# Kernel optimization log

Measured on AMD Instinct MI355X. Metric: run time of the kernel, lower is better.

## Reference

```python
import jax, jax.numpy as jnp
from jax import lax
import numpy as np
jax.config.update("jax_enable_x64", True)

NUM_CLASSES = 4
RADIUS = 3
POOL = 2
HALF_D = RADIUS ** 3  # 27
_CLIP_MIN = 1e-06
_POS_ALPHA = 0.0005


def setup_inputs() -> dict:
    key = jax.random.key(0)
    k1, k2 = jax.random.split(key)
    logits = jax.random.normal(k1, (2, NUM_CLASSES, 96, 96, 96), dtype=jnp.float32)
    labels = jax.random.randint(k2, (2, 96, 96, 96), 0, NUM_CLASSES).astype(jnp.int64)
    return {"logits": logits, "labels": labels}


def _max_pool3d(x):
    # kernel=stride=POOL over the last three dims of [N,C,H,W,Z]
    return lax.reduce_window(x, -jnp.inf, lax.max,
                             (1, 1, POOL, POOL, POOL), (1, 1, POOL, POOL, POOL), 'VALID')


def _get_pair_vectors(x):
    # x: [N,C,H,W,Z] -> [N,C,HALF_D, (H-R+1)*(W-R+1)*(Z-R+1)] of shifted overlapping copies
    n, c, h, w, z = x.shape
    nh, nw, nz = h - (RADIUS - 1), w - (RADIUS - 1), z - (RADIUS - 1)
    shifts = [x[:, :, i:i + nh, j:j + nw, k:k + nz]
              for i in range(RADIUS) for j in range(RADIUS) for k in range(RADIUS)]
    return jnp.stack(shifts, axis=2).reshape(n, c, HALF_D, -1)


def reference(logits, labels):
    mask = (labels < NUM_CLASSES)                     # [N,H,W,Z] bool
    maskf = mask.astype(jnp.float32)
    onehot = jax.nn.one_hot(labels * mask, NUM_CLASSES, dtype=jnp.float32)  # [N,H,W,Z,C]
    onehot = onehot * maskf[..., None]
    onehot = jnp.transpose(onehot, (0, 4, 1, 2, 3))   # [N,C,H,W,Z]
    probs = jax.nn.sigmoid(logits) * maskf[:, None] + _CLIP_MIN

    la = _max_pool3d(onehot)
    pr = _max_pool3d(probs)

    la_v = _get_pair_vectors(la).astype(jnp.float64)  # [N,C,D,M]
    pr_v = _get_pair_vectors(pr).astype(jnp.float64)

    eye = jnp.eye(HALF_D, dtype=jnp.float64)
    la_v = la_v - la_v.mean(axis=3, keepdims=True)
    pr_v = pr_v - pr_v.mean(axis=3, keepdims=True)
    la_cov = jnp.einsum('ncdm,ncem->ncde', la_v, la_v)
    pr_cov = jnp.einsum('ncdm,ncem->ncde', pr_v, pr_v)
    pr_cov_inv = jnp.linalg.inv(pr_cov + eye * _POS_ALPHA)
    la_pr_cov = jnp.einsum('ncdm,ncem->ncde', la_v, pr_v)
    appro_var = la_cov - la_pr_cov @ pr_cov_inv @ jnp.swapaxes(la_pr_cov, -2, -1)

    chol = jnp.linalg.cholesky(appro_var + eye * _POS_ALPHA)
    diag = jnp.diagonal(chol, axis1=-2, axis2=-1)
    rmi_now = 0.5 * 2.0 * jnp.sum(jnp.log(diag + 1e-08), axis=-1)  # [N,C]
    rmi_per_class = rmi_now.reshape(-1, NUM_CLASSES).mean(axis=0).astype(jnp.float32)
    rmi_per_class = rmi_per_class / float(HALF_D)
    return jnp.sum(rmi_per_class)
```

## Files before the change

### kernel.cpp

```cpp
#include <hip/hip_runtime.h>
#include <math.h>

#define NVAL  97336
#define NCH   8

typedef unsigned short u16;
typedef unsigned int u32;
typedef __attribute__((ext_vector_type(8))) short bf16x8;
typedef __attribute__((ext_vector_type(4))) float f32x4;
typedef __attribute__((ext_vector_type(4))) unsigned int u32x4;

#define LINE_B 336
#define COPY_B 112
#define VOL_B  21504
#define GLINE_U16 48

__global__ __launch_bounds__(256) void pool_kernel(
    const float* __restrict__ logits, const int* __restrict__ labels,
    u16* __restrict__ shifted, float* __restrict__ gacc,
    float* __restrict__ out) {
  int t = blockIdx.x * 256 + threadIdx.x;
  if (t == 0) out[0] = 0.0f;
  if (blockIdx.x < 80) gacc[blockIdx.x * 256 + threadIdx.x] = 0.0f;
  if (t >= 2 * 110592) return;
  int Z = t % 48; int tmp = t / 48;
  int Y = tmp % 48; tmp /= 48;
  int X = tmp % 48; int n = tmp / 48;
  int sb = (2 * X) * 9216 + (2 * Y) * 96 + 2 * Z;
  const int2* lb2 = (const int2*)(labels + n * 884736 + sb);
  int2 La = lb2[0], Lb = lb2[48], Lc = lb2[4608], Ld = lb2[4656];
  #pragma unroll
  for (int c = 0; c < 4; c++) {
    const float2* lg2 = (const float2*)(logits + (size_t)(n * 4 + c) * 884736 + sb);
    float2 v0 = lg2[0], v1 = lg2[48], v2 = lg2[4608], v3 = lg2[4656];
    float mx = fmaxf(fmaxf(fmaxf(v0.x, v0.y), fmaxf(v1.x, v1.y)),
                     fmaxf(fmaxf(v2.x, v2.y), fmaxf(v3.x, v3.y)));
    float pr = 1.0f / (1.0f + expf(-mx)) + 1e-6f;
    int la = (La.x == c || La.y == c || Lb.x == c || Lb.y == c ||
              Lc.x == c || Lc.y == c || Ld.x == c || Ld.y == c);
    u16 la16 = la ? (u16)0x3F80 : (u16)0;
    unsigned int u = __float_as_uint(pr);
    u16 pr16 = (u16)((u + 0x7FFF + ((u >> 16) & 1)) >> 16);
    int ch = n * 4 + c;
    shifted[((size_t)(ch * 2 + 0) * 2304 + X * 48 + Y) * GLINE_U16 + Z] = la16;
    shifted[((size_t)(ch * 2 + 1) * 2304 + X * 48 + Y) * GLINE_U16 + Z] = pr16;
  }
}

#define MFMA16(A, B, C) __builtin_amdgcn_mfma_f32_16x16x32_bf16((A), (B), (C), 0, 0, 0)

#define STEP(BA, AM) do {                                                  \
    int _ba = (BA);                                                        \
    u32x4 ub0 = *(const u32x4*)(smem + _ba + laneC0);                      \
    u32x4 ub1 = *(const u32x4*)(smem + _ba + laneC1);                      \
    u32x4 ub2 = *(const u32x4*)(smem + _ba + laneC2);                      \
    u32x4 ub3 = *(const u32x4*)(smem + _ba + laneC3);                      \
    ub3 = iszero ? zer4 : (isones ? one4 : ub3);                           \
    u32x4 ua0 = ub0, ua1 = ub1, ua2 = ub2, ua3 = ub3;                      \
    ua0.w &= (AM); ua1.w &= (AM); ua2.w &= (AM); ua3.w &= (AM);            \
    bf16x8 A0 = __builtin_bit_cast(bf16x8, ua0);                           \
    bf16x8 A1 = __builtin_bit_cast(bf16x8, ua1);                           \
    bf16x8 A2 = __builtin_bit_cast(bf16x8, ua2);                           \
    bf16x8 A3 = __builtin_bit_cast(bf16x8, ua3);                           \
    bf16x8 B0 = __builtin_bit_cast(bf16x8, ub0);                           \
    bf16x8 B1 = __builtin_bit_cast(bf16x8, ub1);                           \
    bf16x8 B2 = __builtin_bit_cast(bf16x8, ub2);                           \
    bf16x8 B3 = __builtin_bit_cast(bf16x8, ub3);                           \
    acc0 = MFMA16(A0, B0, acc0);  acc1 = MFMA16(A0, B1, acc1);             \
    acc2 = MFMA16(A0, B2, acc2);  acc3 = MFMA16(A0, B3, acc3);             \
    acc4 = MFMA16(A1, B1, acc4);  acc5 = MFMA16(A1, B2, acc5);             \
    acc6 = MFMA16(A1, B3, acc6);  acc7 = MFMA16(A2, B2, acc7);             \
    acc8 = MFMA16(A2, B3, acc8);  acc9 = MFMA16(A3, B3, acc9);             \
  } while (0)

__global__ __launch_bounds__(256) void gram_kernel(
    const u16* __restrict__ shifted, float* __restrict__ gacc) {
  __shared__ __align__(16) unsigned char smem[43008];
  int bx = blockIdx.x;
  int ch = bx >> 6, xt = (bx >> 3) & 7, yt = bx & 7;
  int X0 = xt * 6, Y0 = yt * 6;
  int tw = (xt == 7) ? 4 : 6, th = (yt == 7) ? 4 : 6;
  int tid = threadIdx.x;

  const u16* base = shifted + (size_t)ch * 2 * 2304 * GLINE_U16;
  for (int j = tid; j < 768; j += 256) {
    int chunk = j % 6; int li = j / 6;
    int sy = li & 7, sx = (li >> 3) & 7, vol = li >> 6;
    int gx = X0 + sx; if (gx > 47) gx = 47;
    int gy = Y0 + sy; if (gy > 47) gy = 47;
    const u32* src = (const u32*)(base +
        ((size_t)vol * 2304 + gx * 48 + gy) * GLINE_U16);
    u32x4 v = *(const u32x4*)(src + chunk * 4);
    u32 d4 = (chunk < 5) ? src[chunk * 4 + 4] : 0u;
    unsigned char* dst = smem + vol * VOL_B + ((sx << 3) + sy) * LINE_B + chunk * 16;
    *(u32x4*)(dst) = v;
    u32x4 s1 = { (v.x >> 16) | (v.y << 16), (v.y >> 16) | (v.z << 16),
                 (v.z >> 16) | (v.w << 16), (v.w >> 16) | (d4 << 16) };
    *(u32x4*)(dst + COPY_B) = s1;
    u32x4 s2 = { v.y, v.z, v.w, d4 };
    *(u32x4*)(dst + 2 * COPY_B) = s2;
  }
  __syncthreads();

  int lane = tid & 63, w = tid >> 6;
  int q = lane >> 4, rlo = lane & 15;
#define LANEC(F) ({ int _r = (F) * 16 + rlo; int _vol = 0, _s = 0;           \
    if (_r < 27) { _s = _r; } else if (_r < 54) { _vol = 1; _s = _r - 27; }  \
    int _dx = _s / 9, _dy = (_s / 3) % 3, _dz = _s % 3;                      \
    _vol * VOL_B + ((_dx << 3) + _dy) * LINE_B + _dz * COPY_B; })
  int laneC0 = LANEC(0), laneC1 = LANEC(1), laneC2 = LANEC(2), laneC3 = LANEC(3);
  unsigned int am1 = (q == 1) ? 0u : ~0u;
  unsigned int am2 = (q == 3) ? 0u : ~0u;
  bool isones = (rlo == 6);
  bool iszero = (rlo > 6);
  u32x4 one4 = {0x3F803F80u, 0x3F803F80u, 0x3F803F80u, 0x3F803F80u};
  u32x4 zer4 = {0u, 0u, 0u, 0u};

  f32x4 acc0 = {0,0,0,0}, acc1 = {0,0,0,0}, acc2 = {0,0,0,0}, acc3 = {0,0,0,0};
  f32x4 acc4 = {0,0,0,0}, acc5 = {0,0,0,0}, acc6 = {0,0,0,0}, acc7 = {0,0,0,0};
  f32x4 acc8 = {0,0,0,0}, acc9 = {0,0,0,0};

  int npl = (tw * th) >> 1;
  for (int pl = w; pl < npl; pl += 4) {
    int L0 = 2 * pl, L1 = L0 + 1;
    int lx0 = L0 / th, ly0 = L0 - lx0 * th;
    int lx1 = L1 / th, ly1 = L1 - lx1 * th;
    int U0 = ((lx0 << 3) + ly0) * LINE_B;
    int U1 = ((lx1 << 3) + ly1) * LINE_B;
    STEP(U0 + 16 * q, ~0u);
    STEP((q < 2) ? (U0 + 64 + 16 * q) : (U1 + 16 * q - 32), am1);
    STEP(U1 + 32 + 16 * q, am2);
  }
  __syncthreads();

  float* Pf = (float*)smem;
#define FL(T, A) { float* _qp = Pf + w * 2560 + (T) * 256 + lane;            \
    _qp[0] = (A).x; _qp[64] = (A).y; _qp[128] = (A).z; _qp[192] = (A).w; }
  FL(0, acc0) FL(1, acc1) FL(2, acc2) FL(3, acc3) FL(4, acc4)
  FL(5, acc5) FL(6, acc6) FL(7, acc7) FL(8, acc8) FL(9, acc9)
  __syncthreads();
  float* dst = gacc + (size_t)ch * 2560;
  for (int u2 = tid; u2 < 2560; u2 += 256)
    atomicAdd(&dst[u2], Pf[u2] + Pf[u2 + 2560] + Pf[u2 + 5120] + Pf[u2 + 7680]);
}

#define MS 56
__device__ inline double g54(const float* __restrict__ G, int R, int C) {
  int I = R >> 4, J = C >> 4;
  if (I > J) { int tt = R; R = C; C = tt; I = R >> 4; J = C >> 4; }
  int tile = 4 * I - ((I * (I - 1)) >> 1) + (J - I);
  int r = R & 15, c = C & 15;
  return (double)G[tile * 256 + (r & 3) * 64 + ((r >> 2) << 4) + c];
}

__device__ inline int tri_row(int u) {
  int a = (int)((sqrtf(8.0f * (float)u + 1.0f) - 1.0f) * 0.5f);
  while ((a + 1) * (a + 2) / 2 <= u) a++;
  while (a * (a + 1) / 2 > u) a--;
  return a;
}

__global__ __launch_bounds__(256) void stage2_kernel(
    const float* __restrict__ gacc, float* __restrict__ out) {
  __shared__ double M[54 * MS];
  __shared__ double slv[27], spv[27], piv[54], lred[27];
  int ch = blockIdx.x, tid = threadIdx.x;
  const double Minv = 1.0 / (double)NVAL;
  const double alpha = 5e-4;
  const float* G = gacc + (size_t)ch * 2560;

  if (tid < 27) { slv[tid] = g54(G, tid, 54); spv[tid] = g54(G, 27 + tid, 54); }
  __syncthreads();
  for (int u = tid; u < 1485; u += 256) {
    int a = tri_row(u);
    int b = u - a * (a + 1) / 2;
    double v;
    if (a < 27) {
      v = g54(G, 27 + a, 27 + b) - spv[a] * spv[b] * Minv + ((a == b) ? alpha : 0.0);
    } else if (b >= 27) {
      int d = a - 27, e = b - 27;
      v = g54(G, d, e) - slv[d] * slv[e] * Minv + ((d == e) ? alpha : 0.0);
    } else {
      v = g54(G, a - 27, 27 + b) - slv[a - 27] * spv[b] * Minv;
    }
    M[a * MS + b] = v;
  }
  __syncthreads();

  #pragma unroll 1
  for (int phase = 0; phase < 6; phase++) {
    int k0 = phase * 8;
    double P[8][8];
    #pragma unroll
    for (int k = 0; k < 8; k++)
      #pragma unroll
      for (int j = 0; j <= k; j++)
        P[k][j] = M[(k0 + k) * MS + (k0 + j)];
    double idv[8];
    #pragma unroll
    for (int k = 0; k < 8; k++) {
      idv[k] = 1.0 / P[k][k];
      #pragma unroll
      for (int i = k + 1; i < 8; i++) {
        double l = P[i][k] * idv[k];
        #pragma unroll
        for (int j = k + 1; j <= i; j++)
          P[i][j] -= l * P[j][k];
      }
      #pragma unroll
      for (int i = k + 1; i < 8; i++) P[i][k] *= idv[k];
    }
    if (tid == 0) {
      #pragma unroll
      for (int k = 0; k < 8; k++) piv[k0 + k] = P[k][k];
    }
    int base = k0 + 8, n = 54 - base;
    int ncell = n * (n + 1) / 2;
    for (int u = tid; u < ncell; u += 256) {
      int ii = tri_row(u);
      int jj = u - ii * (ii + 1) / 2;
      int i = base + ii, j = base + jj;
      const double2* Ai = (const double2*)(M + i * MS + k0);
      const double2* Bj = (const double2*)(M + j * MS + k0);
      double2 a01 = Ai[0], a23 = Ai[1], a45 = Ai[2], a67 = Ai[3];
      double2 b01 = Bj[0], b23 = Bj[1], b45 = Bj[2], b67 = Bj[3];
      double av[8] = {a01.x, a01.y, a23.x, a23.y, a45.x, a45.y, a67.x, a67.y};
      double bv[8] = {b01.x, b01.y, b23.x, b23.y, b45.x, b45.y, b67.x, b67.y};
      #pragma unroll
      for (int k = 1; k < 8; k++) {
        #pragma unroll
        for (int m = 0; m < k; m++) {
          av[k] -= P[k][m] * av[m];
          bv[k] -= P[k][m] * bv[m];
        }
      }
      double acc = 0.0;
      #pragma unroll
      for (int k = 0; k < 8; k++) acc += av[k] * (bv[k] * idv[k]);
      M[i * MS + j] -= acc;
    }
    __syncthreads();
  }

  if (tid == 0) {
    double T[6][6];
    #pragma unroll
    for (int k = 0; k < 6; k++)
      #pragma unroll
      for (int j = 0; j <= k; j++)
        T[k][j] = M[(48 + k) * MS + (48 + j)];
    #pragma unroll
    for (int k = 0; k < 6; k++) {
      double dk = T[k][k];
      piv[48 + k] = dk;
      double id = 1.0 / dk;
      #pragma unroll
      for (int i = k + 1; i < 6; i++) {
        double l = T[i][k] * id;
        #pragma unroll
        for (int j = k + 1; j <= i; j++)
          T[i][j] -= l * T[j][k];
      }
    }
  }
  __syncthreads();

  if (tid < 27) lred[tid] = log(sqrt(piv[27 + tid]) + 1e-8);
  __syncthreads();
  if (tid == 0) {
    double s = 0.0;
    for (int i = 0; i < 27; i++) s += lred[i];
    atomicAdd(out, (float)(s / 54.0));
  }
}

extern "C" void kernel_launch(void* const* d_in, const int* in_sizes, int n_in,
                              void* d_out, int out_size, void* d_ws, size_t ws_size,
                              hipStream_t stream) {
  const float* logits = (const float*)d_in[0];
  const int* labels = (const int*)d_in[1];
  float* out = (float*)d_out;

  float* gacc = (float*)d_ws;
  u16* shifted = (u16*)((char*)d_ws + 131072);

  pool_kernel<<<864, 256, 0, stream>>>(logits, labels, shifted, gacc, out);
  gram_kernel<<<512, 256, 0, stream>>>(shifted, gacc);
  stage2_kernel<<<NCH, 256, 0, stream>>>(gacc, out);
}
```

Baseline: 102.9 us.

## Fuse stage2 into gram kernel via last-block counter; vectorize pooling to two outputs per thread

The separate stage2 launch is removed. Each gram block bumps a per-channel atomic counter after its accumulation, and the last block for a channel runs the 54x54 factorization in its own shared memory. The pool kernel now handles two Z outputs per thread with float4/int4 loads and packed 32-bit stores, which halves the grid. This saves one kernel launch and widens memory accesses, but adds threadfence and atomic read-back overhead, and the tail work is serialized onto whichever block finishes last.

```diff
diff --git a/kernel.cpp b/kernel.cpp
--- a/kernel.cpp
+++ b/kernel.cpp
@@ -18,32 +18,41 @@
 __global__ __launch_bounds__(256) void pool_kernel(
     const float* __restrict__ logits, const int* __restrict__ labels,
     u16* __restrict__ shifted, float* __restrict__ gacc,
-    float* __restrict__ out) {
+    int* __restrict__ cnt, float* __restrict__ out) {
   int t = blockIdx.x * 256 + threadIdx.x;
   if (t == 0) out[0] = 0.0f;
   if (blockIdx.x < 80) gacc[blockIdx.x * 256 + threadIdx.x] = 0.0f;
-  if (t >= 2 * 110592) return;
-  int Z = t % 48; int tmp = t / 48;
+  if (blockIdx.x == 80 && threadIdx.x < NCH) cnt[threadIdx.x] = 0;
+  int Zp = t % 24; int tmp = t / 24;
   int Y = tmp % 48; tmp /= 48;
   int X = tmp % 48; int n = tmp / 48;
-  int sb = (2 * X) * 9216 + (2 * Y) * 96 + 2 * Z;
-  const int2* lb2 = (const int2*)(labels + n * 884736 + sb);
-  int2 La = lb2[0], Lb = lb2[48], Lc = lb2[4608], Ld = lb2[4656];
+  int sb = (2 * X) * 9216 + (2 * Y) * 96 + 4 * Zp;
+  const int4* lb4 = (const int4*)(labels + n * 884736 + sb);
+  int4 La = lb4[0], Lb = lb4[24], Lc = lb4[2304], Ld = lb4[2328];
   #pragma unroll
   for (int c = 0; c < 4; c++) {
-    const float2* lg2 = (const float2*)(logits + (size_t)(n * 4 + c) * 884736 + sb);
-    float2 v0 = lg2[0], v1 = lg2[48], v2 = lg2[4608], v3 = lg2[4656];
-    float mx = fmaxf(fmaxf(fmaxf(v0.x, v0.y), fmaxf(v1.x, v1.y)),
-                     fmaxf(fmaxf(v2.x, v2.y), fmaxf(v3.x, v3.y)));
-    float pr = 1.0f / (1.0f + expf(-mx)) + 1e-6f;
-    int la = (La.x == c || La.y == c || Lb.x == c || Lb.y == c ||
-              Lc.x == c || Lc.y == c || Ld.x == c || Ld.y == c);
-    u16 la16 = la ? (u16)0x3F80 : (u16)0;
-    unsigned int u = __float_as_uint(pr);
-    u16 pr16 = (u16)((u + 0x7FFF + ((u >> 16) & 1)) >> 16);
+    const float4* lg4 = (const float4*)(logits + (size_t)(n * 4 + c) * 884736 + sb);
+    float4 v0 = lg4[0], v1 = lg4[24], v2 = lg4[2304], v3 = lg4[2328];
+    float mx0 = fmaxf(fmaxf(fmaxf(v0.x, v0.y), fmaxf(v1.x, v1.y)),
+                      fmaxf(fmaxf(v2.x, v2.y), fmaxf(v3.x, v3.y)));
+    float mx1 = fmaxf(fmaxf(fmaxf(v0.z, v0.w), fmaxf(v1.z, v1.w)),
+                      fmaxf(fmaxf(v2.z, v2.w), fmaxf(v3.z, v3.w)));
+    float pr0 = 1.0f / (1.0f + expf(-mx0)) + 1e-6f;
+    float pr1 = 1.0f / (1.0f + expf(-mx1)) + 1e-6f;
+    int la0 = (La.x == c || La.y == c || Lb.x == c || Lb.y == c ||
+               Lc.x == c || Lc.y == c || Ld.x == c || Ld.y == c);
+    int la1 = (La.z == c || La.w == c || Lb.z == c || Lb.w == c ||
+               Lc.z == c || Lc.w == c || Ld.z == c || Ld.w == c);
+    u32 lapack = (la0 ? 0x3F80u : 0u) | (la1 ? 0x3F800000u : 0u);
+    unsigned int q0 = __float_as_uint(pr0);
+    unsigned int q1 = __float_as_uint(pr1);
+    u32 p0 = (q0 + 0x7FFF + ((q0 >> 16) & 1)) >> 16;
+    u32 p1 = (q1 + 0x7FFF + ((q1 >> 16) & 1)) & 0xFFFF0000u;
+    u32 prpack = p0 | p1;
     int ch = n * 4 + c;
-    shifted[((size_t)(ch * 2 + 0) * 2304 + X * 48 + Y) * GLINE_U16 + Z] = la16;
-    shifted[((size_t)(ch * 2 + 1) * 2304 + X * 48 + Y) * GLINE_U16 + Z] = pr16;
+    int line = X * 48 + Y;
+    ((u32*)shifted)[((size_t)(ch * 2 + 0) * 2304 + line) * 24 + Zp] = lapack;
+    ((u32*)shifted)[((size_t)(ch * 2 + 1) * 2304 + line) * 24 + Zp] = prpack;
   }
 }
 
@@ -73,9 +82,28 @@
     acc8 = MFMA16(A2, B3, acc8);  acc9 = MFMA16(A3, B3, acc9);             \
   } while (0)
 
+#define MS 56
+
+__device__ inline double g54(const float* __restrict__ G, int R, int C) {
+  int I = R >> 4, J = C >> 4;
+  if (I > J) { int tt = R; R = C; C = tt; I = R >> 4; J = C >> 4; }
+  int tile = 4 * I - ((I * (I - 1)) >> 1) + (J - I);
+  int r = R & 15, c = C & 15;
+  return (double)G[tile * 256 + (r & 3) * 64 + ((r >> 2) << 4) + c];
+}
+
+__device__ inline int tri_row(int u) {
+  int a = (int)((sqrtf(8.0f * (float)u + 1.0f) - 1.0f) * 0.5f);
+  while ((a + 1) * (a + 2) / 2 <= u) a++;
+  while (a * (a + 1) / 2 > u) a--;
+  return a;
+}
+
 __global__ __launch_bounds__(256) void gram_kernel(
-    const u16* __restrict__ shifted, float* __restrict__ gacc) {
+    const u16* __restrict__ shifted, float* __restrict__ gacc,
+    int* __restrict__ cnt, float* __restrict__ out) {
   __shared__ __align__(16) unsigned char smem[43008];
+  __shared__ int winflag;
   int bx = blockIdx.x;
   int ch = bx >> 6, xt = (bx >> 3) & 7, yt = bx & 7;
   int X0 = xt * 6, Y0 = yt * 6;
@@ -92,13 +120,13 @@
         ((size_t)vol * 2304 + gx * 48 + gy) * GLINE_U16);
     u32x4 v = *(const u32x4*)(src + chunk * 4);
     u32 d4 = (chunk < 5) ? src[chunk * 4 + 4] : 0u;
-    unsigned char* dst = smem + vol * VOL_B + ((sx << 3) + sy) * LINE_B + chunk * 16;
-    *(u32x4*)(dst) = v;
+    unsigned char* dstp = smem + vol * VOL_B + ((sx << 3) + sy) * LINE_B + chunk * 16;
+    *(u32x4*)(dstp) = v;
     u32x4 s1 = { (v.x >> 16) | (v.y << 16), (v.y >> 16) | (v.z << 16),
                  (v.z >> 16) | (v.w << 16), (v.w >> 16) | (d4 << 16) };
-    *(u32x4*)(dst + COPY_B) = s1;
+    *(u32x4*)(dstp + COPY_B) = s1;
     u32x4 s2 = { v.y, v.z, v.w, d4 };
-    *(u32x4*)(dst + 2 * COPY_B) = s2;
+    *(u32x4*)(dstp + 2 * COPY_B) = s2;
   }
   __syncthreads();
 
@@ -142,32 +170,26 @@
   float* dst = gacc + (size_t)ch * 2560;
   for (int u2 = tid; u2 < 2560; u2 += 256)
     atomicAdd(&dst[u2], Pf[u2] + Pf[u2 + 2560] + Pf[u2 + 5120] + Pf[u2 + 7680]);
-}
-
-#define MS 56
-__device__ inline double g54(const float* __restrict__ G, int R, int C) {
-  int I = R >> 4, J = C >> 4;
-  if (I > J) { int tt = R; R = C; C = tt; I = R >> 4; J = C >> 4; }
-  int tile = 4 * I - ((I * (I - 1)) >> 1) + (J - I);
-  int r = R & 15, c = C & 15;
-  return (double)G[tile * 256 + (r & 3) * 64 + ((r >> 2) << 4) + c];
-}
-
-__device__ inline int tri_row(int u) {
-  int a = (int)((sqrtf(8.0f * (float)u + 1.0f) - 1.0f) * 0.5f);
-  while ((a + 1) * (a + 2) / 2 <= u) a++;
-  while (a * (a + 1) / 2 > u) a--;
-  return a;
-}
-
-__global__ __launch_bounds__(256) void stage2_kernel(
-    const float* __restrict__ gacc, float* __restrict__ out) {
-  __shared__ double M[54 * MS];
-  __shared__ double slv[27], spv[27], piv[54], lred[27];
-  int ch = blockIdx.x, tid = threadIdx.x;
+
+  __threadfence();
+  if (tid == 0) winflag = (atomicAdd(&cnt[ch], 1) == 63) ? 1 : 0;
+  __syncthreads();
+  if (!winflag) return;
+  __threadfence();
+
+  double* M = (double*)smem;
+  float* gsf = (float*)(smem + 24192);
+  double* slv = (double*)(smem + 34432);
+  double* spv = (double*)(smem + 34648);
+  double* piv = (double*)(smem + 34864);
+  double* lred = (double*)(smem + 35296);
   const double Minv = 1.0 / (double)NVAL;
   const double alpha = 5e-4;
-  const float* G = gacc + (size_t)ch * 2560;
+
+  for (int u2 = tid; u2 < 2560; u2 += 256)
+    gsf[u2] = atomicAdd(&dst[u2], 0.0f);
+  __syncthreads();
+  const float* G = gsf;
 
   if (tid < 27) { slv[tid] = g54(G, tid, 54); spv[tid] = g54(G, 27 + tid, 54); }
   __syncthreads();
@@ -214,12 +236,12 @@
       #pragma unroll
       for (int k = 0; k < 8; k++) piv[k0 + k] = P[k][k];
     }
-    int base = k0 + 8, n = 54 - base;
+    int bstart = k0 + 8, n = 54 - bstart;
     int ncell = n * (n + 1) / 2;
     for (int u = tid; u < ncell; u += 256) {
       int ii = tri_row(u);
       int jj = u - ii * (ii + 1) / 2;
-      int i = base + ii, j = base + jj;
+      int i = bstart + ii, j = bstart + jj;
       const double2* Ai = (const double2*)(M + i * MS + k0);
       const double2* Bj = (const double2*)(M + j * MS + k0);
       double2 a01 = Ai[0], a23 = Ai[1], a45 = Ai[2], a67 = Ai[3];
@@ -282,9 +304,9 @@
   float* out = (float*)d_out;
 
   float* gacc = (float*)d_ws;
+  int* cnt = (int*)((char*)d_ws + 81920);
   u16* shifted = (u16*)((char*)d_ws + 131072);
 
-  pool_kernel<<<864, 256, 0, stream>>>(logits, labels, shifted, gacc, out);
-  gram_kernel<<<512, 256, 0, stream>>>(shifted, gacc);
-  stage2_kernel<<<NCH, 256, 0, stream>>>(gacc, out);
-}
+  pool_kernel<<<432, 256, 0, stream>>>(logits, labels, shifted, gacc, cnt, out);
+  gram_kernel<<<512, 256, 0, stream>>>(shifted, gacc, cnt, out);
+}
```

After: 130.0 us. 1.26x slower.
